# Performance work log

Measured on AMD Instinct MI355X. Metric: run time of the kernel, lower is better.

Reference implementation:

```python
import jax, jax.numpy as jnp
import numpy as np

N_NODES = 50000
N_EDGES = 800000
N_GRAPHS = 100
IN_DIM = 100
OUT_DIM = 128
N_ETYPES = 4
N_STEPS = 8


def setup_inputs() -> dict:
    key = jax.random.key(0)
    ks = jax.random.split(key, 16)
    s = 0.05
    return {
        "features": jax.random.normal(ks[0], (N_NODES, IN_DIM), jnp.float32),
        "edge_src": jax.random.randint(ks[1], (N_EDGES,), 0, N_NODES, jnp.int32),
        "edge_dst": jax.random.randint(ks[2], (N_EDGES,), 0, N_NODES, jnp.int32),
        "edge_types": jax.random.randint(ks[3], (N_EDGES,), 0, N_ETYPES, jnp.int32),
        "graph_ids": jnp.sort(jax.random.randint(ks[4], (N_NODES,), 0, N_GRAPHS, jnp.int32)),
        "W_msg": jax.random.normal(ks[5], (N_ETYPES, OUT_DIM, OUT_DIM), jnp.float32) * s,
        "b_msg": jax.random.normal(ks[6], (N_ETYPES, OUT_DIM), jnp.float32) * s,
        "W_ih": jax.random.normal(ks[7], (3 * OUT_DIM, OUT_DIM), jnp.float32) * s,
        "W_hh": jax.random.normal(ks[8], (3 * OUT_DIM, OUT_DIM), jnp.float32) * s,
        "b_ih": jax.random.normal(ks[9], (3 * OUT_DIM,), jnp.float32) * s,
        "b_hh": jax.random.normal(ks[10], (3 * OUT_DIM,), jnp.float32) * s,
        "W1": jax.random.normal(ks[11], (256, OUT_DIM), jnp.float32) * s,
        "b1": jax.random.normal(ks[12], (256,), jnp.float32) * s,
        "W2": jax.random.normal(ks[13], (1, 256), jnp.float32) * s,
        "b2": jax.random.normal(ks[14], (1,), jnp.float32) * s,
    }


def _gru_cell(x, h, W_ih, W_hh, b_ih, b_hh):
    # torch.nn.GRUCell: gate order (reset, update, new)
    gi = x @ W_ih.T + b_ih  # [N, 3D]
    gh = h @ W_hh.T + b_hh
    i_r, i_z, i_n = jnp.split(gi, 3, axis=-1)
    h_r, h_z, h_n = jnp.split(gh, 3, axis=-1)
    r = jax.nn.sigmoid(i_r + h_r)
    z = jax.nn.sigmoid(i_z + h_z)
    n = jnp.tanh(i_n + r * h_n)
    return (1.0 - z) * n + z * h


def reference(features, edge_src, edge_dst, edge_types, graph_ids,
              W_msg, b_msg, W_ih, W_hh, b_ih, b_hh, W1, b1, W2, b2):
    n_nodes = features.shape[0]
    # DGL GatedGraphConv: zero-pad input features to out_feats
    h = jnp.pad(features, ((0, 0), (0, OUT_DIM - features.shape[1])))
    for _ in range(N_STEPS):
        # per-edge-type linear transform of source features: [T, N, D]
        transformed = jnp.einsum('nd,tdf->tnf', h, W_msg) + b_msg[:, None, :]
        msgs = transformed[edge_types, edge_src]  # [E, D] gather
        a = jax.ops.segment_sum(msgs, edge_dst, num_segments=n_nodes)  # scatter-add
        h = _gru_cell(a, h, W_ih, W_hh, b_ih, b_hh)
    # masked mean pooling per graph (mask_mean over de-batchified graphs)
    counts = jax.ops.segment_sum(jnp.ones((n_nodes,), h.dtype), graph_ids,
                                 num_segments=N_GRAPHS)
    sums = jax.ops.segment_sum(h, graph_ids, num_segments=N_GRAPHS)
    pooled = sums / jnp.maximum(counts, 1.0)[:, None]  # [B, D]
    # classifier: Linear -> relu -> (dropout: eval noop) -> Linear -> sigmoid
    hidden = jax.nn.relu(pooled @ W1.T + b1)
    logits = hidden @ W2.T + b2  # [B, 1]
    return jax.nn.sigmoid(logits).squeeze(-1)  # [B]
```

## Files before the change

kernel.cpp:

```cpp
#include <hip/hip_runtime.h>
#include <hip/hip_bf16.h>
#include <math.h>

#define N_NODES 50000
#define M_PAD   50048
#define N_EDGES 800000
#define N_GRAPHS 100
#define IN_DIM 100
#define D 128
#define N_STEPS 8
#define NBINS (N_NODES * 4)
#define SCAN_BLOCKS 196

typedef unsigned short ushort_t;
typedef __bf16 bf16x8 __attribute__((ext_vector_type(8)));
typedef float f32x4 __attribute__((ext_vector_type(4)));

__device__ inline ushort_t f2b(float f) {
  __hip_bfloat16 b = __float2bfloat16(f);
  return *reinterpret_cast<ushort_t*>(&b);
}
__device__ inline float b2f(unsigned int u16) {
  unsigned int x = u16 << 16;
  return __builtin_bit_cast(float, x);
}

__device__ __attribute__((always_inline)) inline void gld16(const ushort_t* g, ushort_t* l) {
  __builtin_amdgcn_global_load_lds(
      (const __attribute__((address_space(1))) void*)g,
      (__attribute__((address_space(3))) void*)l, 16, 0, 0);
}

__global__ void pad_cast_kernel(const float* __restrict__ feat, ushort_t* __restrict__ h) {
  int idx = blockIdx.x * blockDim.x + threadIdx.x;
  if (idx >= N_NODES * D) return;
  int n = idx >> 7, d = idx & 127;
  float v = (d < IN_DIM) ? feat[n * IN_DIM + d] : 0.0f;
  h[(size_t)n * 128 + d] = f2b(v);
}

__global__ void prep_bts(const float* __restrict__ W_msg, ushort_t* __restrict__ BtS) {
  int idx = blockIdx.x * blockDim.x + threadIdx.x;
  if (idx >= 128 * 512) return;
  int f = idx >> 9, kp = idx & 511;
  int t = kp >> 7, k = kp & 127;
  BtS[(size_t)f * 512 + kp] = f2b(W_msg[((size_t)t * 128 + k) * 128 + f]);
}

__global__ void prep_wg(const float* __restrict__ W_ih, const float* __restrict__ W_hh,
                        const float* __restrict__ b_ih, const float* __restrict__ b_hh,
                        ushort_t* __restrict__ WgT, float* __restrict__ gbias) {
  int idx = blockIdx.x * blockDim.x + threadIdx.x;
  if (idx >= 512 * 256) return;
  int colp = idx >> 8, k = idx & 255;
  int g = colp >> 6, gate = (colp >> 4) & 3, r = colp & 15;
  int d = g * 16 + r;
  float v;
  if (gate == 3)      v = (k < 128) ? 0.f : W_hh[(size_t)(256 + d) * 128 + (k - 128)];
  else if (gate == 2) v = (k < 128) ? W_ih[(size_t)(256 + d) * 128 + k] : 0.f;
  else {
    int j0 = (gate == 0) ? d : 128 + d;
    v = (k < 128) ? W_ih[(size_t)j0 * 128 + k] : W_hh[(size_t)j0 * 128 + (k - 128)];
  }
  WgT[(size_t)colp * 256 + k] = f2b(v);
  if (k == 0) {
    float bb = (gate == 0) ? b_ih[d] + b_hh[d]
             : (gate == 1) ? b_ih[128 + d] + b_hh[128 + d]
             : (gate == 2) ? b_ih[256 + d] : b_hh[256 + d];
    gbias[colp] = bb;
  }
}

__global__ void hist_kernel(const int* __restrict__ edst, const int* __restrict__ etype,
                            int* __restrict__ cnt2, int* __restrict__ rank) {
  int e = blockIdx.x * 256 + threadIdx.x;
  if (e >= N_EDGES) return;
  rank[e] = atomicAdd(&cnt2[edst[e] * 4 + etype[e]], 1);
}

__global__ __launch_bounds__(1024) void scanA(const int* __restrict__ cnt2,
                                              int* __restrict__ tmp, int* __restrict__ bsum) {
  __shared__ int wsum[16];
  int b = blockIdx.x, t = threadIdx.x;
  int i = b * 1024 + t;
  int lane = t & 63, wid = t >> 6;
  int x = (i < NBINS) ? cnt2[i] : 0;
  #pragma unroll
  for (int s = 1; s < 64; s <<= 1) {
    int y = __shfl_up(x, s, 64);
    if (lane >= s) x += y;
  }
  if (lane == 63) wsum[wid] = x;
  __syncthreads();
  if (wid == 0) {
    int w = (lane < 16) ? wsum[lane] : 0;
    #pragma unroll
    for (int s = 1; s < 16; s <<= 1) {
      int y = __shfl_up(w, s, 64);
      if (lane >= s) w += y;
    }
    if (lane < 16) wsum[lane] = w;
  }
  __syncthreads();
  int wb = (wid > 0) ? wsum[wid - 1] : 0;
  tmp[i] = wb + x;
  if (t == 1023) bsum[b] = wsum[15];
}

__global__ __launch_bounds__(64) void scanB(const int* __restrict__ bsum,
                                            int* __restrict__ bpre) {
  int lane = threadIdx.x;
  int carry = 0;
  for (int base = 0; base < SCAN_BLOCKS; base += 64) {
    int idx = base + lane;
    int v = (idx < SCAN_BLOCKS) ? bsum[idx] : 0;
    int x = v;
    #pragma unroll
    for (int s = 1; s < 64; s <<= 1) {
      int y = __shfl_up(x, s, 64);
      if (lane >= s) x += y;
    }
    if (idx < SCAN_BLOCKS) bpre[idx] = carry + x - v;
    carry += __shfl(x, 63, 64);
  }
}

__global__ __launch_bounds__(1024) void scanC(const int* __restrict__ tmp,
                                              const int* __restrict__ bpre,
                                              int* __restrict__ offs2) {
  int b = blockIdx.x, t = threadIdx.x;
  int i = b * 1024 + t;
  if (i < NBINS) offs2[i + 1] = tmp[i] + bpre[b];
  if (i == 0) offs2[0] = 0;
}

__global__ void fill_kernel(const int* __restrict__ esrc, const int* __restrict__ edst,
                            const int* __restrict__ etype, const int* __restrict__ offs2,
                            const int* __restrict__ rank, int* __restrict__ payload) {
  int e = blockIdx.x * 256 + threadIdx.x;
  if (e >= N_EDGES) return;
  int key = edst[e] * 4 + etype[e];
  payload[offs2[key] + rank[e]] = esrc[e];
}

__global__ __launch_bounds__(256) void gather_kernel(const int* __restrict__ offs2,
    const int* __restrict__ payload, const ushort_t* __restrict__ hb,
    ushort_t* __restrict__ S, float* __restrict__ cntf) {
  int n = blockIdx.x * 4 + (threadIdx.x >> 6);
  int lane = threadIdx.x & 63;
  if (n >= N_NODES) return;
  int bb[5];
  #pragma unroll
  for (int k = 0; k < 5; ++k) bb[k] = offs2[n * 4 + k];
  float a[4][2] = {{0.f, 0.f}, {0.f, 0.f}, {0.f, 0.f}, {0.f, 0.f}};
  const ushort_t* hrow = hb + lane * 2;
  for (int base = bb[0]; base < bb[4]; base += 64) {
    int lim = min(bb[4], base + 64);
    int cnt = lim - base;
    int pe = (lane < cnt) ? payload[base + lane] : 0;
    #pragma unroll
    for (int t = 0; t < 4; ++t) {
      int lo = max(bb[t], base), hi = min(bb[t + 1], lim);
      int i = lo;
      for (; i + 4 <= hi; i += 4) {
        int s0 = __shfl(pe, i - base, 64);
        int s1 = __shfl(pe, i + 1 - base, 64);
        int s2 = __shfl(pe, i + 2 - base, 64);
        int s3 = __shfl(pe, i + 3 - base, 64);
        unsigned int u0 = *(const unsigned int*)(hrow + (size_t)s0 * 128);
        unsigned int u1 = *(const unsigned int*)(hrow + (size_t)s1 * 128);
        unsigned int u2 = *(const unsigned int*)(hrow + (size_t)s2 * 128);
        unsigned int u3 = *(const unsigned int*)(hrow + (size_t)s3 * 128);
        a[t][0] += b2f(u0 & 0xffff) + b2f(u1 & 0xffff) + b2f(u2 & 0xffff) + b2f(u3 & 0xffff);
        a[t][1] += b2f(u0 >> 16) + b2f(u1 >> 16) + b2f(u2 >> 16) + b2f(u3 >> 16);
      }
      for (; i < hi; ++i) {
        int s0 = __shfl(pe, i - base, 64);
        unsigned int u0 = *(const unsigned int*)(hrow + (size_t)s0 * 128);
        a[t][0] += b2f(u0 & 0xffff);
        a[t][1] += b2f(u0 >> 16);
      }
    }
  }
  #pragma unroll
  for (int t = 0; t < 4; ++t) {
    unsigned int packed = (unsigned int)f2b(a[t][0]) | ((unsigned int)f2b(a[t][1]) << 16);
    *(unsigned int*)(S + (size_t)n * 512 + t * 128 + lane * 2) = packed;
    if (lane == 0) cntf[n * 4 + t] = (float)(bb[t + 1] - bb[t]);
  }
}

__global__ __launch_bounds__(256) void mfma_msg(
    const ushort_t* __restrict__ S,
    const ushort_t* __restrict__ Bt,
    const float* __restrict__ b_msg, const float* __restrict__ cntf,
    ushort_t* __restrict__ a_out) {
  constexpr int K = 512;
  constexpr int NT  = K / 32;
  constexpr int PRE = 3;
  constexpr int SLOT = 12288;
  __shared__ __align__(16) unsigned char smem[SLOT * 4];
  const int m0 = blockIdx.x * 64;
  int tid = threadIdx.x;
  int wave = tid >> 6, lane = tid & 63;
  int wm = (wave & 1) * 32, wn = (wave >> 1) * 64;
  int quad = lane >> 4, l16 = lane & 15;

  int sr = lane >> 2, sc = lane & 3;
  const ushort_t* gA  = S  + (size_t)(m0 + wave * 16 + sr) * K + sc * 8;
  const ushort_t* gB0 = Bt + (size_t)(wave * 32 + sr) * K + sc * 8;
  const ushort_t* gB1 = gB0 + (size_t)16 * K;

  auto stage = [&](int slot, int t) {
    ushort_t* base = (ushort_t*)(smem + slot * SLOT);
    int k0 = t * 32;
    gld16(gA + k0,  base + wave * 512);
    gld16(gB0 + k0, base + 2048 + wave * 1024);
    gld16(gB1 + k0, base + 2048 + wave * 1024 + 512);
  };

  f32x4 acc[2][4];
  #pragma unroll
  for (int i = 0; i < 2; ++i)
    #pragma unroll
    for (int j = 0; j < 4; ++j) acc[i][j] = (f32x4){0.f, 0.f, 0.f, 0.f};

  #pragma unroll
  for (int t = 0; t < PRE; ++t) stage(t, t);

  #pragma unroll
  for (int t = 0; t < NT; ++t) {
    int infl = NT - 1 - t;
    if (infl >= 2)      asm volatile("s_waitcnt vmcnt(6) lgkmcnt(0)" ::: "memory");
    else if (infl == 1) asm volatile("s_waitcnt vmcnt(3) lgkmcnt(0)" ::: "memory");
    else                asm volatile("s_waitcnt vmcnt(0) lgkmcnt(0)" ::: "memory");
    __builtin_amdgcn_s_barrier();
    if (t + PRE < NT) stage((t + PRE) & 3, t + PRE);
    const ushort_t* As = (const ushort_t*)(smem + (t & 3) * SLOT);
    const ushort_t* Bs = As + 2048;
    bf16x8 af[2], bfr[4];
    #pragma unroll
    for (int i = 0; i < 2; ++i) af[i] = *(const bf16x8*)&As[(wm + i * 16 + l16) * 32 + quad * 8];
    #pragma unroll
    for (int j = 0; j < 4; ++j) bfr[j] = *(const bf16x8*)&Bs[(wn + j * 16 + l16) * 32 + quad * 8];
    #pragma unroll
    for (int i = 0; i < 2; ++i)
      #pragma unroll
      for (int j = 0; j < 4; ++j)
        acc[i][j] = __builtin_amdgcn_mfma_f32_16x16x32_bf16(af[i], bfr[j], acc[i][j], 0, 0, 0);
  }

  ushort_t* Ep = (ushort_t*)smem;
  float bm[4][4];
  #pragma unroll
  for (int j = 0; j < 4; ++j)
    #pragma unroll
    for (int t = 0; t < 4; ++t)
      bm[j][t] = b_msg[t * 128 + wn + j * 16 + l16];
  #pragma unroll
  for (int p = 0; p < 2; ++p) {
    if (p) __syncthreads();
    #pragma unroll
    for (int reg = 0; reg < 4; ++reg) {
      int slot = (wm >> 5) * 16 + quad * 4 + reg;
      int m = m0 + wm + p * 16 + quad * 4 + reg;
      float4 c = *(const float4*)(cntf + (size_t)m * 4);
      #pragma unroll
      for (int j = 0; j < 4; ++j) {
        float val = acc[p][j][reg] + c.x * bm[j][0] + c.y * bm[j][1]
                                   + c.z * bm[j][2] + c.w * bm[j][3];
        Ep[slot * 136 + wn + j * 16 + l16] = f2b(val);
      }
    }
    __syncthreads();
    #pragma unroll
    for (int c2 = 0; c2 < 2; ++c2) {
      int chunk = tid + 256 * c2;
      int slot = chunk >> 4, sub = chunk & 15;
      int m = m0 + (slot & 15) + (slot >> 4) * 32 + p * 16;
      *(uint4*)(a_out + (size_t)m * 128 + sub * 8) =
          *(const uint4*)&Ep[slot * 136 + sub * 8];
    }
  }
}

__global__ __launch_bounds__(256) void mfma_gru(
    const ushort_t* __restrict__ Aa, const ushort_t* __restrict__ Ah,
    const ushort_t* __restrict__ Bt,
    const float* __restrict__ bias,
    ushort_t* __restrict__ h_out) {
  constexpr int K = 256;
  constexpr int NT  = K / 32;
  constexpr int PRE = 3;
  constexpr int SLOT = 12288;
  __shared__ __align__(16) unsigned char smem[SLOT * 4];
  const int m0 = blockIdx.x * 64, n0 = blockIdx.y * 128;
  int tid = threadIdx.x;
  int wave = tid >> 6, lane = tid & 63;
  int wm = (wave & 1) * 32, wn = (wave >> 1) * 64;
  int quad = lane >> 4, l16 = lane & 15;

  int sr = lane >> 2, sc = lane & 3;
  const ushort_t* gAa = Aa + (size_t)(m0 + wave * 16 + sr) * 128 + sc * 8;
  const ushort_t* gAh = Ah + (size_t)(m0 + wave * 16 + sr) * 128 + sc * 8;
  const ushort_t* gB0 = Bt + (size_t)(n0 + wave * 32 + sr) * K   + sc * 8;
  const ushort_t* gB1 = gB0 + (size_t)16 * K;

  auto stage = [&](int slot, int t) {
    ushort_t* base = (ushort_t*)(smem + slot * SLOT);
    const ushort_t* srcA = (t < 4) ? (gAa + t * 32) : (gAh + (t - 4) * 32);
    gld16(srcA, base + wave * 512);
    gld16(gB0 + t * 32, base + 2048 + wave * 1024);
    gld16(gB1 + t * 32, base + 2048 + wave * 1024 + 512);
  };

  f32x4 acc[2][4];
  #pragma unroll
  for (int i = 0; i < 2; ++i)
    #pragma unroll
    for (int j = 0; j < 4; ++j) acc[i][j] = (f32x4){0.f, 0.f, 0.f, 0.f};

  #pragma unroll
  for (int t = 0; t < PRE; ++t) stage(t, t);

  #pragma unroll
  for (int t = 0; t < NT; ++t) {
    int infl = NT - 1 - t;
    if (infl >= 2)      asm volatile("s_waitcnt vmcnt(6) lgkmcnt(0)" ::: "memory");
    else if (infl == 1) asm volatile("s_waitcnt vmcnt(3) lgkmcnt(0)" ::: "memory");
    else                asm volatile("s_waitcnt vmcnt(0) lgkmcnt(0)" ::: "memory");
    __builtin_amdgcn_s_barrier();
    if (t + PRE < NT) stage((t + PRE) & 3, t + PRE);
    const ushort_t* As = (const ushort_t*)(smem + (t & 3) * SLOT);
    const ushort_t* Bs = As + 2048;
    bf16x8 af[2], bfr[4];
    #pragma unroll
    for (int i = 0; i < 2; ++i) af[i] = *(const bf16x8*)&As[(wm + i * 16 + l16) * 32 + quad * 8];
    #pragma unroll
    for (int j = 0; j < 4; ++j) bfr[j] = *(const bf16x8*)&Bs[(wn + j * 16 + l16) * 32 + quad * 8];
    #pragma unroll
    for (int i = 0; i < 2; ++i)
      #pragma unroll
      for (int j = 0; j < 4; ++j)
        acc[i][j] = __builtin_amdgcn_mfma_f32_16x16x32_bf16(af[i], bfr[j], acc[i][j], 0, 0, 0);
  }

  ushort_t* Ap = (ushort_t*)smem;
  int db = (n0 >> 6) * 16;
  int dim_loc = (wn >> 6) * 16 + l16;
  float br = bias[n0 + wn + l16];
  float bz = bias[n0 + wn + 16 + l16];
  float bi = bias[n0 + wn + 32 + l16];
  float bh = bias[n0 + wn + 48 + l16];
  #pragma unroll
  for (int i = 0; i < 2; ++i)
    #pragma unroll
    for (int reg = 0; reg < 4; ++reg) {
      int r_loc = wm + i * 16 + quad * 4 + reg;
      int m = m0 + r_loc;
      float pr  = acc[i][0][reg] + br;
      float pz  = acc[i][1][reg] + bz;
      float in_ = acc[i][2][reg] + bi;
      float hn  = acc[i][3][reg] + bh;
      float r = 1.0f / (1.0f + expf(-pr));
      float z = 1.0f / (1.0f + expf(-pz));
      float nn = tanhf(in_ + r * hn);
      float hold = b2f(Ah[(size_t)m * 128 + db + dim_loc]);
      float hv = (1.0f - z) * nn + z * hold;
      Ap[r_loc * 40 + dim_loc] = f2b(hv);
    }
  __syncthreads();
  {
    int row = tid >> 2, sub = tid & 3;
    *(uint4*)(h_out + (size_t)(m0 + row) * 128 + db + sub * 8) =
        *(const uint4*)&Ap[row * 40 + sub * 8];
  }
}

__global__ __launch_bounds__(128) void pool_kernel(const ushort_t* __restrict__ h,
    const int* __restrict__ gids, float* __restrict__ pooled, float* __restrict__ gcnt) {
  __shared__ int lo_s, hi_s;
  int g = blockIdx.x, c = blockIdx.y, d = threadIdx.x;
  if (d == 0) {
    int lo = 0, hi = N_NODES;
    while (lo < hi) { int mid = (lo + hi) >> 1; if (gids[mid] < g) lo = mid + 1; else hi = mid; }
    lo_s = lo;
    int lo2 = lo, hi2 = N_NODES;
    while (lo2 < hi2) { int mid = (lo2 + hi2) >> 1; if (gids[mid] < g + 1) lo2 = mid + 1; else hi2 = mid; }
    hi_s = lo2;
  }
  __syncthreads();
  int lo = lo_s, hi = hi_s;
  int len = hi - lo;
  int b = lo + (int)(((long long)len * c) >> 3);
  int e = lo + (int)(((long long)len * (c + 1)) >> 3);
  float s = 0.f;
  for (int n = b; n < e; ++n) s += b2f(h[(size_t)n * 128 + d]);
  if (e > b) atomicAdd(&pooled[g * 128 + d], s);
  if (c == 0 && d == 0) gcnt[g] = (float)len;
}

__global__ __launch_bounds__(256) void classifier_kernel(
    const float* __restrict__ pooled, const float* __restrict__ gcnt,
    const float* __restrict__ W1, const float* __restrict__ b1,
    const float* __restrict__ W2, const float* __restrict__ b2,
    float* __restrict__ out) {
  __shared__ float p[D];
  __shared__ float hid[256];
  __shared__ float wsum[4];
  int g = blockIdx.x;
  int t = threadIdx.x;
  float cnt = fmaxf(gcnt[g], 1.0f);
  if (t < D) p[t] = pooled[g * D + t] / cnt;
  __syncthreads();
  float acc = b1[t];
  const float* w = W1 + (size_t)t * D;
  for (int k = 0; k < D; ++k) acc += p[k] * w[k];
  hid[t] = fmaxf(acc, 0.0f);
  __syncthreads();
  float v = hid[t] * W2[t];
  for (int off = 32; off > 0; off >>= 1) v += __shfl_down(v, off, 64);
  if ((t & 63) == 0) wsum[t >> 6] = v;
  __syncthreads();
  if (t == 0) {
    float s = wsum[0] + wsum[1] + wsum[2] + wsum[3] + b2[0];
    out[g] = 1.0f / (1.0f + expf(-s));
  }
}

extern "C" void kernel_launch(void* const* d_in, const int* in_sizes, int n_in,
                              void* d_out, int out_size, void* d_ws, size_t ws_size,
                              hipStream_t stream) {
  const float* features = (const float*)d_in[0];
  const int* esrc  = (const int*)d_in[1];
  const int* edst  = (const int*)d_in[2];
  const int* etype = (const int*)d_in[3];
  const int* gids  = (const int*)d_in[4];
  const float* W_msg = (const float*)d_in[5];
  const float* b_msg = (const float*)d_in[6];
  const float* W_ih  = (const float*)d_in[7];
  const float* W_hh  = (const float*)d_in[8];
  const float* b_ih  = (const float*)d_in[9];
  const float* b_hh  = (const float*)d_in[10];
  const float* W1 = (const float*)d_in[11];
  const float* b1 = (const float*)d_in[12];
  const float* W2 = (const float*)d_in[13];
  const float* b2 = (const float*)d_in[14];
  float* out = (float*)d_out;

  char* ws = (char*)d_ws;
  size_t off_b = 0;
  auto alloc = [&](size_t bytes) -> void* {
    void* p = ws + off_b;
    off_b += (bytes + 255) & ~(size_t)255;
    return p;
  };
  ushort_t* hA     = (ushort_t*)alloc((size_t)M_PAD * 128 * 2);
  ushort_t* hB     = (ushort_t*)alloc((size_t)M_PAD * 128 * 2);
  ushort_t* aArr   = (ushort_t*)alloc((size_t)M_PAD * 128 * 2);
  ushort_t* S      = (ushort_t*)alloc((size_t)M_PAD * 512 * 2);
  float*    cntf   = (float*)alloc((size_t)M_PAD * 4 * 4);
  ushort_t* BtS    = (ushort_t*)alloc(128 * 512 * 2);
  ushort_t* WgT    = (ushort_t*)alloc(512 * 256 * 2);
  float*    gbias  = (float*)alloc(512 * 4);
  int*      cnt2   = (int*)alloc((size_t)NBINS * 4);
  int*      offs2  = (int*)alloc((size_t)(NBINS + 1) * 4);
  int*      rank   = (int*)alloc((size_t)N_EDGES * 4);
  int*      tmp    = (int*)alloc((size_t)SCAN_BLOCKS * 1024 * 4);
  int*      bsum   = (int*)alloc(SCAN_BLOCKS * 4);
  int*      bpre   = (int*)alloc(SCAN_BLOCKS * 4);
  int*      payload= (int*)alloc((size_t)N_EDGES * 4);
  float*    pooled = (float*)alloc(N_GRAPHS * 128 * 4);
  float*    gcnt   = (float*)alloc(N_GRAPHS * 4);

  pad_cast_kernel<<<(N_NODES * 128 + 255) / 256, 256, 0, stream>>>(features, hA);
  prep_bts<<<(128 * 512 + 255) / 256, 256, 0, stream>>>(W_msg, BtS);
  prep_wg<<<(512 * 256 + 255) / 256, 256, 0, stream>>>(W_ih, W_hh, b_ih, b_hh, WgT, gbias);
  hipMemsetAsync(cnt2, 0, (size_t)NBINS * 4, stream);
  hist_kernel<<<(N_EDGES + 255) / 256, 256, 0, stream>>>(edst, etype, cnt2, rank);
  scanA<<<SCAN_BLOCKS, 1024, 0, stream>>>(cnt2, tmp, bsum);
  scanB<<<1, 64, 0, stream>>>(bsum, bpre);
  scanC<<<SCAN_BLOCKS, 1024, 0, stream>>>(tmp, bpre, offs2);
  fill_kernel<<<(N_EDGES + 255) / 256, 256, 0, stream>>>(esrc, edst, etype, offs2, rank, payload);

  ushort_t* hc = hA;
  ushort_t* hn = hB;
  for (int step = 0; step < N_STEPS; ++step) {
    gather_kernel<<<(N_NODES + 3) / 4, 256, 0, stream>>>(offs2, payload, hc, S, cntf);
    mfma_msg<<<M_PAD / 64, 256, 0, stream>>>(S, BtS, b_msg, cntf, aArr);
    mfma_gru<<<dim3(M_PAD / 64, 4), 256, 0, stream>>>(aArr, hc, WgT, gbias, hn);
    ushort_t* t2 = hc; hc = hn; hn = t2;
  }

  hipMemsetAsync(pooled, 0, (size_t)N_GRAPHS * 128 * 4, stream);
  pool_kernel<<<dim3(N_GRAPHS, 8), 128, 0, stream>>>(hc, gids, pooled, gcnt);
  classifier_kernel<<<N_GRAPHS, 256, 0, stream>>>(pooled, gcnt, W1, b1, W2, b2, out);
}
```

Baseline: 917.6 us.

## Fuse message GEMM and GRU GEMM into one kernel via LDS-resident tiles

Merges the message-transform GEMM and the GRU gate GEMM into a single kernel per 64-row tile. The aggregated message and the old hidden state stay in XOR-swizzled LDS instead of going through a global intermediate, and the GRU weights are read straight from global memory with no LDS staging. This drops one kernel launch per step and the write and re-read of the intermediate array. In exchange each block now handles all four gate column chunks serially, giving a quarter as many blocks in the GRU phase, and the weight loads are unpipelined.

After: 1.140 ms. 24.3% more time.

```diff
diff --git a/kernel.cpp b/kernel.cpp
--- a/kernel.cpp
+++ b/kernel.cpp
@@ -190,16 +190,22 @@
   }
 }
 
-__global__ __launch_bounds__(256) void mfma_msg(
+__global__ __launch_bounds__(256) void fused_msg_gru(
     const ushort_t* __restrict__ S,
     const ushort_t* __restrict__ Bt,
+    const ushort_t* __restrict__ Hc,
+    const ushort_t* __restrict__ Wg,
     const float* __restrict__ b_msg, const float* __restrict__ cntf,
-    ushort_t* __restrict__ a_out) {
+    const float* __restrict__ gbias,
+    ushort_t* __restrict__ h_out) {
   constexpr int K = 512;
   constexpr int NT  = K / 32;
   constexpr int PRE = 3;
   constexpr int SLOT = 12288;
   __shared__ __align__(16) unsigned char smem[SLOT * 4];
+  char* aT = (char*)smem;
+  char* hT = (char*)smem + 16384;
+  char* oT = (char*)smem + 32768;
   const int m0 = blockIdx.x * 64;
   int tid = threadIdx.x;
   int wave = tid >> 6, lane = tid & 63;
@@ -250,130 +256,96 @@
         acc[i][j] = __builtin_amdgcn_mfma_f32_16x16x32_bf16(af[i], bfr[j], acc[i][j], 0, 0, 0);
   }
 
-  ushort_t* Ep = (ushort_t*)smem;
-  float bm[4][4];
-  #pragma unroll
-  for (int j = 0; j < 4; ++j)
-    #pragma unroll
-    for (int t = 0; t < 4; ++t)
-      bm[j][t] = b_msg[t * 128 + wn + j * 16 + l16];
-  #pragma unroll
-  for (int p = 0; p < 2; ++p) {
-    if (p) __syncthreads();
-    #pragma unroll
-    for (int reg = 0; reg < 4; ++reg) {
-      int slot = (wm >> 5) * 16 + quad * 4 + reg;
-      int m = m0 + wm + p * 16 + quad * 4 + reg;
-      float4 c = *(const float4*)(cntf + (size_t)m * 4);
+  {
+    float bm[4][4];
+    #pragma unroll
+    for (int j = 0; j < 4; ++j)
+      #pragma unroll
+      for (int t = 0; t < 4; ++t)
+        bm[j][t] = b_msg[t * 128 + wn + j * 16 + l16];
+    #pragma unroll
+    for (int i = 0; i < 2; ++i)
+      #pragma unroll
+      for (int reg = 0; reg < 4; ++reg) {
+        int row = wm + i * 16 + quad * 4 + reg;
+        float4 c = *(const float4*)(cntf + (size_t)(m0 + row) * 4);
+        #pragma unroll
+        for (int j = 0; j < 4; ++j) {
+          float val = acc[i][j][reg] + c.x * bm[j][0] + c.y * bm[j][1]
+                                     + c.z * bm[j][2] + c.w * bm[j][3];
+          int col = wn + j * 16 + l16;
+          *(ushort_t*)(aT + ((row * 256 + col * 2) ^ ((row & 7) << 4))) = f2b(val);
+        }
+      }
+  }
+  #pragma unroll
+  for (int c4 = 0; c4 < 4; ++c4) {
+    int r = wave * 16 + c4 * 4 + (lane >> 4);
+    const ushort_t* src = Hc + (size_t)(m0 + r) * 128 + (((lane & 15) ^ (r & 7)) * 8);
+    gld16(src, (ushort_t*)(hT + (wave * 16 + c4 * 4) * 256));
+  }
+  asm volatile("s_waitcnt vmcnt(0) lgkmcnt(0)" ::: "memory");
+  __builtin_amdgcn_s_barrier();
+
+  for (int c = 0; c < 4; ++c) {
+    f32x4 pacc[2][4];
+    #pragma unroll
+    for (int i = 0; i < 2; ++i)
+      #pragma unroll
+      for (int j = 0; j < 4; ++j) pacc[i][j] = (f32x4){0.f, 0.f, 0.f, 0.f};
+    #pragma unroll
+    for (int t = 0; t < 8; ++t) {
+      const char* tile = (t < 4) ? aT : hT;
+      int kb = (t & 3) * 64;
+      bf16x8 af2[2], bfr2[4];
+      #pragma unroll
+      for (int i = 0; i < 2; ++i) {
+        int row = wm + i * 16 + l16;
+        af2[i] = *(const bf16x8*)(tile + ((row * 256 + quad * 16 + kb) ^ ((row & 7) << 4)));
+      }
       #pragma unroll
       for (int j = 0; j < 4; ++j) {
-        float val = acc[p][j][reg] + c.x * bm[j][0] + c.y * bm[j][1]
-                                   + c.z * bm[j][2] + c.w * bm[j][3];
-        Ep[slot * 136 + wn + j * 16 + l16] = f2b(val);
-      }
+        int colp = c * 128 + wn + j * 16 + l16;
+        bfr2[j] = *(const bf16x8*)(Wg + (size_t)colp * 256 + t * 32 + quad * 8);
+      }
+      #pragma unroll
+      for (int i = 0; i < 2; ++i)
+        #pragma unroll
+        for (int j = 0; j < 4; ++j)
+          pacc[i][j] = __builtin_amdgcn_mfma_f32_16x16x32_bf16(af2[i], bfr2[j], pacc[i][j], 0, 0, 0);
     }
-    __syncthreads();
-    #pragma unroll
-    for (int c2 = 0; c2 < 2; ++c2) {
-      int chunk = tid + 256 * c2;
-      int slot = chunk >> 4, sub = chunk & 15;
-      int m = m0 + (slot & 15) + (slot >> 4) * 32 + p * 16;
-      *(uint4*)(a_out + (size_t)m * 128 + sub * 8) =
-          *(const uint4*)&Ep[slot * 136 + sub * 8];
+    int db = c * 32 + (wave >> 1) * 16;
+    float br = gbias[c * 128 + wn + l16];
+    float bz = gbias[c * 128 + wn + 16 + l16];
+    float bi = gbias[c * 128 + wn + 32 + l16];
+    float bh = gbias[c * 128 + wn + 48 + l16];
+    #pragma unroll
+    for (int i = 0; i < 2; ++i)
+      #pragma unroll
+      for (int reg = 0; reg < 4; ++reg) {
+        int row = wm + i * 16 + quad * 4 + reg;
+        float pr  = pacc[i][0][reg] + br;
+        float pz  = pacc[i][1][reg] + bz;
+        float in_ = pacc[i][2][reg] + bi;
+        float hn  = pacc[i][3][reg] + bh;
+        float r = 1.0f / (1.0f + expf(-pr));
+        float z = 1.0f / (1.0f + expf(-pz));
+        float nn = tanhf(in_ + r * hn);
+        int hb_off = (row * 256 + (db + l16) * 2) ^ ((row & 7) << 4);
+        float hold = b2f(*(const ushort_t*)(hT + hb_off));
+        float hv = (1.0f - z) * nn + z * hold;
+        *(ushort_t*)(oT + hb_off) = f2b(hv);
+      }
+  }
+  __syncthreads();
+  {
+    int row = tid >> 2, q = tid & 3;
+    #pragma unroll
+    for (int ci = 0; ci < 4; ++ci) {
+      int byte_ = (row * 256 + q * 64 + ci * 16) ^ ((row & 7) << 4);
+      uint4 v = *(const uint4*)(oT + byte_);
+      *(uint4*)(h_out + (size_t)(m0 + row) * 128 + q * 32 + ci * 8) = v;
     }
-  }
-}
-
-__global__ __launch_bounds__(256) void mfma_gru(
-    const ushort_t* __restrict__ Aa, const ushort_t* __restrict__ Ah,
-    const ushort_t* __restrict__ Bt,
-    const float* __restrict__ bias,
-    ushort_t* __restrict__ h_out) {
-  constexpr int K = 256;
-  constexpr int NT  = K / 32;
-  constexpr int PRE = 3;
-  constexpr int SLOT = 12288;
-  __shared__ __align__(16) unsigned char smem[SLOT * 4];
-  const int m0 = blockIdx.x * 64, n0 = blockIdx.y * 128;
-  int tid = threadIdx.x;
-  int wave = tid >> 6, lane = tid & 63;
-  int wm = (wave & 1) * 32, wn = (wave >> 1) * 64;
-  int quad = lane >> 4, l16 = lane & 15;
-
-  int sr = lane >> 2, sc = lane & 3;
-  const ushort_t* gAa = Aa + (size_t)(m0 + wave * 16 + sr) * 128 + sc * 8;
-  const ushort_t* gAh = Ah + (size_t)(m0 + wave * 16 + sr) * 128 + sc * 8;
-  const ushort_t* gB0 = Bt + (size_t)(n0 + wave * 32 + sr) * K   + sc * 8;
-  const ushort_t* gB1 = gB0 + (size_t)16 * K;
-
-  auto stage = [&](int slot, int t) {
-    ushort_t* base = (ushort_t*)(smem + slot * SLOT);
-    const ushort_t* srcA = (t < 4) ? (gAa + t * 32) : (gAh + (t - 4) * 32);
-    gld16(srcA, base + wave * 512);
-    gld16(gB0 + t * 32, base + 2048 + wave * 1024);
-    gld16(gB1 + t * 32, base + 2048 + wave * 1024 + 512);
-  };
-
-  f32x4 acc[2][4];
-  #pragma unroll
-  for (int i = 0; i < 2; ++i)
-    #pragma unroll
-    for (int j = 0; j < 4; ++j) acc[i][j] = (f32x4){0.f, 0.f, 0.f, 0.f};
-
-  #pragma unroll
-  for (int t = 0; t < PRE; ++t) stage(t, t);
-
-  #pragma unroll
-  for (int t = 0; t < NT; ++t) {
-    int infl = NT - 1 - t;
-    if (infl >= 2)      asm volatile("s_waitcnt vmcnt(6) lgkmcnt(0)" ::: "memory");
-    else if (infl == 1) asm volatile("s_waitcnt vmcnt(3) lgkmcnt(0)" ::: "memory");
-    else                asm volatile("s_waitcnt vmcnt(0) lgkmcnt(0)" ::: "memory");
-    __builtin_amdgcn_s_barrier();
-    if (t + PRE < NT) stage((t + PRE) & 3, t + PRE);
-    const ushort_t* As = (const ushort_t*)(smem + (t & 3) * SLOT);
-    const ushort_t* Bs = As + 2048;
-    bf16x8 af[2], bfr[4];
-    #pragma unroll
-    for (int i = 0; i < 2; ++i) af[i] = *(const bf16x8*)&As[(wm + i * 16 + l16) * 32 + quad * 8];
-    #pragma unroll
-    for (int j = 0; j < 4; ++j) bfr[j] = *(const bf16x8*)&Bs[(wn + j * 16 + l16) * 32 + quad * 8];
-    #pragma unroll
-    for (int i = 0; i < 2; ++i)
-      #pragma unroll
-      for (int j = 0; j < 4; ++j)
-        acc[i][j] = __builtin_amdgcn_mfma_f32_16x16x32_bf16(af[i], bfr[j], acc[i][j], 0, 0, 0);
-  }
-
-  ushort_t* Ap = (ushort_t*)smem;
-  int db = (n0 >> 6) * 16;
-  int dim_loc = (wn >> 6) * 16 + l16;
-  float br = bias[n0 + wn + l16];
-  float bz = bias[n0 + wn + 16 + l16];
-  float bi = bias[n0 + wn + 32 + l16];
-  float bh = bias[n0 + wn + 48 + l16];
-  #pragma unroll
-  for (int i = 0; i < 2; ++i)
-    #pragma unroll
-    for (int reg = 0; reg < 4; ++reg) {
-      int r_loc = wm + i * 16 + quad * 4 + reg;
-      int m = m0 + r_loc;
-      float pr  = acc[i][0][reg] + br;
-      float pz  = acc[i][1][reg] + bz;
-      float in_ = acc[i][2][reg] + bi;
-      float hn  = acc[i][3][reg] + bh;
-      float r = 1.0f / (1.0f + expf(-pr));
-      float z = 1.0f / (1.0f + expf(-pz));
-      float nn = tanhf(in_ + r * hn);
-      float hold = b2f(Ah[(size_t)m * 128 + db + dim_loc]);
-      float hv = (1.0f - z) * nn + z * hold;
-      Ap[r_loc * 40 + dim_loc] = f2b(hv);
-    }
-  __syncthreads();
-  {
-    int row = tid >> 2, sub = tid & 3;
-    *(uint4*)(h_out + (size_t)(m0 + row) * 128 + db + sub * 8) =
-        *(const uint4*)&Ap[row * 40 + sub * 8];
   }
 }
 
@@ -457,7 +429,6 @@
   };
   ushort_t* hA     = (ushort_t*)alloc((size_t)M_PAD * 128 * 2);
   ushort_t* hB     = (ushort_t*)alloc((size_t)M_PAD * 128 * 2);
-  ushort_t* aArr   = (ushort_t*)alloc((size_t)M_PAD * 128 * 2);
   ushort_t* S      = (ushort_t*)alloc((size_t)M_PAD * 512 * 2);
   float*    cntf   = (float*)alloc((size_t)M_PAD * 4 * 4);
   ushort_t* BtS    = (ushort_t*)alloc(128 * 512 * 2);
@@ -487,8 +458,8 @@
   ushort_t* hn = hB;
   for (int step = 0; step < N_STEPS; ++step) {
     gather_kernel<<<(N_NODES + 3) / 4, 256, 0, stream>>>(offs2, payload, hc, S, cntf);
-    mfma_msg<<<M_PAD / 64, 256, 0, stream>>>(S, BtS, b_msg, cntf, aArr);
-    mfma_gru<<<dim3(M_PAD / 64, 4), 256, 0, stream>>>(aArr, hc, WgT, gbias, hn);
+    fused_msg_gru<<<M_PAD / 64, 256, 0, stream>>>(
+        S, BtS, hc, WgT, b_msg, cntf, gbias, hn);
     ushort_t* t2 = hc; hc = hn; hn = t2;
   }
 
```
